# Kernel optimization log

Measured on AMD Instinct MI355X. Metric: run time of the kernel, lower is better.

Reference implementation:

```python
import jax, jax.numpy as jnp
import numpy as np

NUM_HEADS = 16

def setup_inputs() -> dict:
    key = jax.random.key(0)
    ks = jax.random.split(key, 5)
    B, N, C = 2, 2048, 1024
    x = jax.random.normal(ks[0], (B, N, C), dtype=jnp.float32)
    s_in = 1.0 / np.sqrt(C)
    Wq = jax.random.normal(ks[1], (C, 2 * C), dtype=jnp.float32) * s_in
    Wk = jax.random.normal(ks[2], (C, 2 * C), dtype=jnp.float32) * s_in
    Wv = jax.random.normal(ks[3], (C, 2 * C), dtype=jnp.float32) * s_in
    Wo = jax.random.normal(ks[4], (2 * C, C), dtype=jnp.float32) * (1.0 / np.sqrt(2 * C))
    return {"x": x, "Wq": Wq, "Wk": Wk, "Wv": Wv, "Wo": Wo}

def reference(x, Wq, Wk, Wv, Wo):
    B, N, C = x.shape
    H = NUM_HEADS
    hd = C // H  # head_dim
    def proj(W):
        # [B,N,2C] -> [B,H,N,2*hd]
        return (x @ W).reshape(B, N, H, 2 * hd).transpose(0, 2, 1, 3)
    q = proj(Wq)
    k = proj(Wk)
    v = proj(Wv)
    q_r, q_i = q[..., :hd], q[..., hd:]
    k_r, k_i = k[..., :hd], k[..., hd:]
    v_r, v_i = v[..., :hd], v[..., hd:]
    # complex inner product real part: Re(Q K^H) = q_r.k_r + q_i.k_i
    scores = (jnp.einsum('bhnd,bhmd->bhnm', q_r, k_r)
              + jnp.einsum('bhnd,bhmd->bhnm', q_i, k_i)) / jnp.sqrt(jnp.float32(hd))
    causal = jnp.tril(jnp.ones((N, N), dtype=bool))  # [N,N]
    scores = jnp.where(causal[None, None], scores, -jnp.inf)
    probs = jax.nn.softmax(scores, axis=-1)  # dropout off (eval mode)
    out_r = jnp.einsum('bhnm,bhmd->bhnd', probs, v_r)
    out_i = jnp.einsum('bhnm,bhmd->bhnd', probs, v_i)
    out = jnp.concatenate([out_r, out_i], axis=-1)  # [B,H,N,2*hd]
    out = out.transpose(0, 2, 1, 3).reshape(B, N, 2 * C)
    return out @ Wo  # [B,N,C]
```

## Files before the change

kernel.cpp:

```cpp
#include <hip/hip_runtime.h>
#include <hip/hip_bf16.h>
#include <stdint.h>
#include <cmath>

using bf16 = __hip_bfloat16;
typedef __attribute__((ext_vector_type(8))) short bf16x8;
typedef __attribute__((ext_vector_type(4))) short bf16x4;
typedef __attribute__((ext_vector_type(4))) float f32x4;

#define MFMA16(a, b, c) __builtin_amdgcn_mfma_f32_16x16x32_bf16(a, b, c, 0, 0, 0)

#if defined(__has_builtin)
#if __has_builtin(__builtin_amdgcn_mfma_f32_16x16x16bf16_1k)
#define HAVE_MFMA_K16 1
#endif
#if __has_builtin(__builtin_amdgcn_exp2f)
#define EXP2F __builtin_amdgcn_exp2f
#endif
#endif
#ifndef HAVE_MFMA_K16
#define HAVE_MFMA_K16 0
#endif
#ifndef EXP2F
#define EXP2F exp2f
#endif

#define NEG_BIG (-1e30f)
#define K2SCALE 0.18033688011112042f

__device__ __forceinline__ short f2bf(float v) {
  return __builtin_bit_cast(short, __float2bfloat16(v));
}

__device__ __forceinline__ f32x4 pv_mfma(bf16x4 va, bf16x4 pb, f32x4 c) {
#if HAVE_MFMA_K16
  return __builtin_amdgcn_mfma_f32_16x16x16bf16_1k(va, pb, c, 0, 0, 0);
#else
  const bf16x8 a = {va[0], va[1], va[2], va[3], 0, 0, 0, 0};
  const bf16x8 b = {pb[0], pb[1], pb[2], pb[3], 0, 0, 0, 0};
  return MFMA16(a, b, c);
#endif
}

__device__ __forceinline__ void async_ld16(const bf16* g, bf16* l) {
  __builtin_amdgcn_global_load_lds(
      (const __attribute__((address_space(1))) unsigned int*)g,
      (__attribute__((address_space(3))) unsigned int*)l, 16, 0, 0);
}

template <typename T> __device__ __forceinline__ T cvt_out(float v);
template <> __device__ __forceinline__ float cvt_out<float>(float v) { return v; }
template <> __device__ __forceinline__ bf16 cvt_out<bf16>(float v) { return __float2bfloat16(v); }

__global__ void prep(const float* __restrict__ x,
                     const float* __restrict__ Wq, const float* __restrict__ Wk,
                     const float* __restrict__ Wv, const float* __restrict__ Wo,
                     bf16* __restrict__ xb, bf16* __restrict__ tq,
                     bf16* __restrict__ tk, bf16* __restrict__ tv,
                     bf16* __restrict__ to_) {
  __shared__ bf16 tile[32][33];
  const int bid = blockIdx.x;
  if (bid < 8192) {
    const int z = bid >> 11, tt = bid & 2047;
    const float* in = z == 0 ? Wq : z == 1 ? Wk : z == 2 ? Wv : Wo;
    bf16* out = z == 0 ? tq : z == 1 ? tk : z == 2 ? tv : to_;
    int R, Cc, c0, r0;
    if (z < 3) { R = 1024; Cc = 2048; c0 = (tt & 63) * 32; r0 = (tt >> 6) * 32; }
    else       { R = 2048; Cc = 1024; c0 = (tt & 31) * 32; r0 = (tt >> 5) * 32; }
    const int xx = threadIdx.x & 31;
    const int y = threadIdx.x >> 5;
#pragma unroll
    for (int yy = y; yy < 32; yy += 8)
      tile[yy][xx] = __float2bfloat16(in[(size_t)(r0 + yy) * Cc + c0 + xx]);
    __syncthreads();
#pragma unroll
    for (int yy = y; yy < 32; yy += 8)
      out[(size_t)(c0 + yy) * R + r0 + xx] = tile[xx][yy];
  } else {
    const int i = (bid - 8192) * 256 + threadIdx.x;
    const float4 v = ((const float4*)x)[i];
    bf16 o[4] = {__float2bfloat16(v.x), __float2bfloat16(v.y),
                 __float2bfloat16(v.z), __float2bfloat16(v.w)};
    *(uint64_t*)&xb[i * 4] = *(const uint64_t*)o;
  }
}

__global__ __launch_bounds__(256)
void gemm_qkv(const bf16* __restrict__ xb, const bf16* __restrict__ wq,
              const bf16* __restrict__ wk, const bf16* __restrict__ wv,
              bf16* __restrict__ qo, bf16* __restrict__ ko, bf16* __restrict__ vo) {
  __shared__ __align__(16) bf16 As[128 * 64];
  __shared__ __align__(16) bf16 Bs[128 * 64];
  const int op = blockIdx.y;
  const int bid = blockIdx.x;
  const bf16 *A, *B;
  int m0, n0;
  if (op < 2) { A = xb; B = op ? wk : wq; m0 = (bid >> 4) * 128; n0 = (bid & 15) * 128; }
  else        { A = wv; B = xb;           m0 = (bid & 15) * 128; n0 = (bid >> 4) * 128; }
  const int K = 1024;

  const int t = threadIdx.x;
  const int l = t & 63, w = t >> 6;
  const int q4 = l >> 4, li = l & 15;
  const int wr = (w >> 1) * 64, wc = (w & 1) * 64;

  f32x4 acc[4][4] = {};
  const int srow = t >> 3;
  const int schu = t & 7;
  const int wavebase = (t & ~63) * 8;
  const bf16* gA = A + (size_t)m0 * K;
  const bf16* gB = B + (size_t)n0 * K;

  for (int k0 = 0; k0 < K; k0 += 64) {
#pragma unroll
    for (int p = 0; p < 4; ++p) {
      const int row = p * 32 + srow;
      const int cs = (schu ^ (row & 7)) * 8;
      const int lbase = p * 2048 + wavebase;
      async_ld16(gA + (size_t)row * K + k0 + cs, &As[lbase]);
      async_ld16(gB + (size_t)row * K + k0 + cs, &Bs[lbase]);
    }
    __syncthreads();
#pragma unroll
    for (int kk = 0; kk < 2; ++kk) {
      bf16x8 af[4], bfr[4];
#pragma unroll
      for (int i = 0; i < 4; ++i)
        af[i] = *(const bf16x8*)&As[(wr + i * 16 + li) * 64 +
                                    (((kk * 4 + q4) ^ (li & 7)) * 8)];
#pragma unroll
      for (int j = 0; j < 4; ++j)
        bfr[j] = *(const bf16x8*)&Bs[(wc + j * 16 + li) * 64 +
                                     (((kk * 4 + q4) ^ (li & 7)) * 8)];
#pragma unroll
      for (int i = 0; i < 4; ++i)
#pragma unroll
        for (int j = 0; j < 4; ++j)
          acc[i][j] = MFMA16(af[i], bfr[j], acc[i][j]);
    }
    __syncthreads();
  }

#pragma unroll
  for (int i = 0; i < 4; ++i)
#pragma unroll
    for (int j = 0; j < 4; ++j)
#pragma unroll
      for (int r = 0; r < 4; ++r) {
        const int gm = m0 + wr + i * 16 + q4 * 4 + r;
        const int gn = n0 + wc + j * 16 + li;
        const bf16 v = __float2bfloat16(acc[i][j][r]);
        if (op < 2) {
          const int b = gm >> 11, nn = gm & 2047;
          const int h = gn >> 7, d = gn & 127;
          (op ? ko : qo)[((size_t)(b * 16 + h) * 2048 + nn) * 128 + d] = v;
        } else {
          const int h = gm >> 7, d = gm & 127;
          const int b = gn >> 11, nn = gn & 2047;
          vo[((size_t)(b * 16 + h) * 128 + d) * 2048 + nn] = v;
        }
      }
}

template <int NT, typename OT>
__global__ __launch_bounds__(256)
void gemm_bt(const bf16* __restrict__ A, const bf16* __restrict__ B,
             OT* __restrict__ C, int M, int N, int K) {
  __shared__ __align__(16) bf16 As[128 * 32];
  __shared__ __align__(16) bf16 Bs[NT * 32];
  constexpr int JN = NT / 32;
  const int t = threadIdx.x;
  const int l = t & 63, w = t >> 6;
  const int q4 = l >> 4, li = l & 15;
  const int m0 = blockIdx.y * 128;
  const int n0 = blockIdx.x * NT;
  const int wr = (w >> 1) * 64, wc = (w & 1) * (NT / 2);

  f32x4 acc[4][JN] = {};
  const int colst = (t & 3) * 8;
  const bf16* gA = A + (size_t)m0 * K;
  const bf16* gB = B + (size_t)n0 * K;

  for (int k0 = 0; k0 < K; k0 += 32) {
#pragma unroll
    for (int p = 0; p < 2; ++p) {
      const int row = p * 64 + (t >> 2);
      const int lbase = p * 2048 + (t & ~63) * 8;
      async_ld16(gA + (size_t)row * K + k0 + colst, &As[lbase]);
    }
#pragma unroll
    for (int p = 0; p < NT / 64; ++p) {
      const int row = p * 64 + (t >> 2);
      const int lbase = p * 2048 + (t & ~63) * 8;
      async_ld16(gB + (size_t)row * K + k0 + colst, &Bs[lbase]);
    }
    __syncthreads();
    bf16x8 af[4], bfr[JN];
#pragma unroll
    for (int i = 0; i < 4; ++i)
      af[i] = *(const bf16x8*)&As[(wr + i * 16 + li) * 32 + q4 * 8];
#pragma unroll
    for (int j = 0; j < JN; ++j)
      bfr[j] = *(const bf16x8*)&Bs[(wc + j * 16 + li) * 32 + q4 * 8];
#pragma unroll
    for (int i = 0; i < 4; ++i)
#pragma unroll
      for (int j = 0; j < JN; ++j)
        acc[i][j] = MFMA16(af[i], bfr[j], acc[i][j]);
    __syncthreads();
  }

#pragma unroll
  for (int i = 0; i < 4; ++i)
#pragma unroll
    for (int j = 0; j < JN; ++j)
#pragma unroll
      for (int r = 0; r < 4; ++r) {
        const int gm = m0 + wr + i * 16 + q4 * 4 + r;
        const int gn = n0 + wc + j * 16 + li;
        C[(size_t)gm * N + gn] = cvt_out<OT>(acc[i][j][r]);
      }
}

__global__ __launch_bounds__(256, 2)
void flash_attn(const bf16* __restrict__ qm, const bf16* __restrict__ km,
                const bf16* __restrict__ vtm, bf16* __restrict__ om) {
  __shared__ __align__(16) bf16 Ks[64 * 128];
  __shared__ __align__(16) bf16 Vts[128 * 64];

  const int t = threadIdx.x;
  const int l = t & 63, w = t >> 6;
  const int q4 = l >> 4, li = l & 15;
  const int bh = blockIdx.x;
  const int y = blockIdx.y;
  const int qt = (y < 16) ? 31 - y : y - 16;
  const int qs = qt * 64;
  const size_t qkbase = (size_t)bh * 2048 * 128;
  const size_t vbase = (size_t)bh * 128 * 2048;
  const int b = bh >> 4, h = bh & 15;

  bf16x8 qf[4];
  {
    const bf16* Qb = qm + qkbase + (size_t)(qs + w * 16 + li) * 128;
#pragma unroll
    for (int f = 0; f < 4; ++f)
      qf[f] = *(const bf16x8*)(Qb + f * 32 + q4 * 8);
  }

  f32x4 O[8] = {};
  float mrun = NEG_BIG, lrun = 0.f;
  const int gmq = qs + w * 16 + li;

  const int ksrow = t >> 4;
  const int kchu = t & 15;
  const int vsrow = t >> 3;
  const int vchu = t & 7;
  const int wavebase = (t & ~63) * 8;

  const int nt = qt + 1;

  for (int j = 0; j < nt; ++j) {
    const int kb = j * 64;
#pragma unroll
    for (int p = 0; p < 4; ++p) {
      const int kr = p * 16 + ksrow;
      async_ld16(km + qkbase + (size_t)(kb + kr) * 128 + (size_t)((kchu ^ (kr & 7)) * 8),
                 &Ks[p * 2048 + wavebase]);
      const int vr = p * 32 + vsrow;
      async_ld16(vtm + vbase + (size_t)vr * 2048 + kb + (size_t)((vchu ^ (vr & 7)) * 8),
                 &Vts[p * 2048 + wavebase]);
    }
    __syncthreads();

    const bool msk = (j == qt);

    f32x4 S[4];
    __builtin_amdgcn_s_setprio(1);
#pragma unroll
    for (int jk = 0; jk < 4; ++jk) {
      const int krow = jk * 16 + li;
      bf16x8 kf[4];
#pragma unroll
      for (int f = 0; f < 4; ++f)
        kf[f] = *(const bf16x8*)&Ks[krow * 128 + (((f * 4 + q4) ^ (li & 7)) * 8)];
      f32x4 s = {0.f, 0.f, 0.f, 0.f};
#pragma unroll
      for (int f = 0; f < 4; ++f) s = MFMA16(kf[f], qf[f], s);
      S[jk] = s;
    }
    __builtin_amdgcn_s_setprio(0);

    if (msk) {
#pragma unroll
      for (int jk = 0; jk < 4; ++jk)
#pragma unroll
        for (int r = 0; r < 4; ++r)
          if ((kb + jk * 16 + q4 * 4 + r) > gmq) S[jk][r] = NEG_BIG;
    }

    float mx = NEG_BIG;
#pragma unroll
    for (int jk = 0; jk < 4; ++jk)
      mx = fmaxf(mx, fmaxf(fmaxf(S[jk][0], S[jk][1]), fmaxf(S[jk][2], S[jk][3])));
    mx = fmaxf(mx, __shfl_xor(mx, 16));
    mx = fmaxf(mx, __shfl_xor(mx, 32));
    const float mold = mrun;
    const float nm = fmaxf(mrun, mx);
    const bool nomove = (mx <= mold);
    mrun = nm;
    const float nmk = nm * K2SCALE;

    bf16x4 pb[4];
    float rs = 0.f;
#pragma unroll
    for (int jk = 0; jk < 4; ++jk) {
      float e[4];
#pragma unroll
      for (int r = 0; r < 4; ++r) {
        e[r] = EXP2F(__builtin_fmaf(S[jk][r], K2SCALE, -nmk));
        pb[jk][r] = f2bf(e[r]);
      }
      rs += (e[0] + e[1]) + (e[2] + e[3]);
    }
    rs += __shfl_xor(rs, 16);
    rs += __shfl_xor(rs, 32);

    if (__all(nomove)) {
      lrun += rs;
    } else {
      const float alpha = EXP2F((mold - nm) * K2SCALE);
      lrun = lrun * alpha + rs;
#pragma unroll
      for (int dt = 0; dt < 8; ++dt) O[dt] *= alpha;
    }

    __builtin_amdgcn_s_setprio(1);
#pragma unroll
    for (int dt = 0; dt < 8; ++dt)
#pragma unroll
      for (int kc = 0; kc < 4; ++kc) {
        const int gc = kc * 2 + (q4 >> 1);
        const bf16x4 va = *(const bf16x4*)&Vts[(dt * 16 + li) * 64 +
                                               ((gc ^ (li & 7)) * 8) +
                                               (q4 & 1) * 4];
        O[dt] = pv_mfma(va, pb[kc], O[dt]);
      }
    __builtin_amdgcn_s_setprio(0);
    __syncthreads();
  }

  {
    const float inv = 1.0f / lrun;
    const size_t orow = (size_t)(b * 2048 + qs + w * 16 + li) * 2048 + h * 128;
#pragma unroll
    for (int dt = 0; dt < 8; ++dt) {
      bf16x4 o4;
#pragma unroll
      for (int r = 0; r < 4; ++r) o4[r] = f2bf(O[dt][r] * inv);
      *(bf16x4*)&om[orow + dt * 16 + q4 * 4] = o4;
    }
  }
}

extern "C" void kernel_launch(void* const* d_in, const int* in_sizes, int n_in,
                              void* d_out, int out_size, void* d_ws, size_t ws_size,
                              hipStream_t stream) {
  const float* x = (const float*)d_in[0];
  const float* Wq = (const float*)d_in[1];
  const float* Wk = (const float*)d_in[2];
  const float* Wv = (const float*)d_in[3];
  const float* Wo = (const float*)d_in[4];
  float* out = (float*)d_out;

  bf16* ws = (bf16*)d_ws;
  const size_t MEG = 1u << 20;
  bf16* xb = ws;
  bf16* wTq = ws + 4 * MEG;
  bf16* wTk = ws + 6 * MEG;
  bf16* wTv = ws + 8 * MEG;
  bf16* woT = ws + 10 * MEG;
  bf16* at_ws = ws + 2 * MEG;
  bf16* q_ws = ws + 12 * MEG;
  bf16* k_ws = ws + 20 * MEG;
  bf16* vt_ws = ws + 28 * MEG;

  const dim3 blk(256);

  prep<<<dim3(12288), blk, 0, stream>>>(x, Wq, Wk, Wv, Wo, xb, wTq, wTk, wTv, woT);
  gemm_qkv<<<dim3(512, 3), blk, 0, stream>>>(xb, wTq, wTk, wTv, q_ws, k_ws, vt_ws);
  flash_attn<<<dim3(32, 32), blk, 0, stream>>>(q_ws, k_ws, vt_ws, at_ws);
  gemm_bt<64, float><<<dim3(16, 32), blk, 0, stream>>>(at_ws, woT, out, 4096, 1024, 2048);
}
```

Measured before the change: 266.2 us.

## Double K-tile depth in gemm_bt with XOR-swizzled LDS and vectorize prep transpose

The output GEMM kernel now stages 64-wide K slices instead of 32, which halves the number of barrier pairs per K loop. It also XOR-swizzles the 16-byte chunks in LDS to avoid bank conflicts on the fragment reads. The weight-transpose prep kernel now loads float2 and stores packed pairs of bf16 values, so each thread handles two elements. The cost is double the LDS footprint for gemm_bt, which may reduce occupancy.

New measurement: 254.8 us. 1.04x faster.

```diff
diff --git a/kernel.cpp b/kernel.cpp
--- a/kernel.cpp
+++ b/kernel.cpp
@@ -67,15 +67,21 @@
     int R, Cc, c0, r0;
     if (z < 3) { R = 1024; Cc = 2048; c0 = (tt & 63) * 32; r0 = (tt >> 6) * 32; }
     else       { R = 2048; Cc = 1024; c0 = (tt & 31) * 32; r0 = (tt >> 5) * 32; }
-    const int xx = threadIdx.x & 31;
-    const int y = threadIdx.x >> 5;
-#pragma unroll
-    for (int yy = y; yy < 32; yy += 8)
-      tile[yy][xx] = __float2bfloat16(in[(size_t)(r0 + yy) * Cc + c0 + xx]);
-    __syncthreads();
-#pragma unroll
-    for (int yy = y; yy < 32; yy += 8)
-      out[(size_t)(c0 + yy) * R + r0 + xx] = tile[xx][yy];
+    const int xx = threadIdx.x & 15;
+    const int y = threadIdx.x >> 4;
+#pragma unroll
+    for (int yy = y; yy < 32; yy += 16) {
+      const float2 v = *(const float2*)&in[(size_t)(r0 + yy) * Cc + c0 + 2 * xx];
+      tile[yy][2 * xx] = __float2bfloat16(v.x);
+      tile[yy][2 * xx + 1] = __float2bfloat16(v.y);
+    }
+    __syncthreads();
+#pragma unroll
+    for (int yy = y; yy < 32; yy += 16) {
+      short o2[2] = {__builtin_bit_cast(short, tile[2 * xx][yy]),
+                     __builtin_bit_cast(short, tile[2 * xx + 1][yy])};
+      *(uint32_t*)&out[(size_t)(c0 + yy) * R + r0 + 2 * xx] = *(const uint32_t*)o2;
+    }
   } else {
     const int i = (bid - 8192) * 256 + threadIdx.x;
     const float4 v = ((const float4*)x)[i];
@@ -166,8 +172,8 @@
 __global__ __launch_bounds__(256)
 void gemm_bt(const bf16* __restrict__ A, const bf16* __restrict__ B,
              OT* __restrict__ C, int M, int N, int K) {
-  __shared__ __align__(16) bf16 As[128 * 32];
-  __shared__ __align__(16) bf16 Bs[NT * 32];
+  __shared__ __align__(16) bf16 As[128 * 64];
+  __shared__ __align__(16) bf16 Bs[NT * 64];
   constexpr int JN = NT / 32;
   const int t = threadIdx.x;
   const int l = t & 63, w = t >> 6;
@@ -177,36 +183,43 @@
   const int wr = (w >> 1) * 64, wc = (w & 1) * (NT / 2);
 
   f32x4 acc[4][JN] = {};
-  const int colst = (t & 3) * 8;
+  const int srow = t >> 3;
+  const int schu = t & 7;
+  const int wavebase = (t & ~63) * 8;
   const bf16* gA = A + (size_t)m0 * K;
   const bf16* gB = B + (size_t)n0 * K;
 
-  for (int k0 = 0; k0 < K; k0 += 32) {
-#pragma unroll
-    for (int p = 0; p < 2; ++p) {
-      const int row = p * 64 + (t >> 2);
-      const int lbase = p * 2048 + (t & ~63) * 8;
-      async_ld16(gA + (size_t)row * K + k0 + colst, &As[lbase]);
-    }
-#pragma unroll
-    for (int p = 0; p < NT / 64; ++p) {
-      const int row = p * 64 + (t >> 2);
-      const int lbase = p * 2048 + (t & ~63) * 8;
-      async_ld16(gB + (size_t)row * K + k0 + colst, &Bs[lbase]);
-    }
-    __syncthreads();
-    bf16x8 af[4], bfr[JN];
-#pragma unroll
-    for (int i = 0; i < 4; ++i)
-      af[i] = *(const bf16x8*)&As[(wr + i * 16 + li) * 32 + q4 * 8];
-#pragma unroll
-    for (int j = 0; j < JN; ++j)
-      bfr[j] = *(const bf16x8*)&Bs[(wc + j * 16 + li) * 32 + q4 * 8];
-#pragma unroll
-    for (int i = 0; i < 4; ++i)
+  for (int k0 = 0; k0 < K; k0 += 64) {
+#pragma unroll
+    for (int p = 0; p < 4; ++p) {
+      const int row = p * 32 + srow;
+      const int cs = (schu ^ (row & 7)) * 8;
+      async_ld16(gA + (size_t)row * K + k0 + cs, &As[p * 2048 + wavebase]);
+    }
+#pragma unroll
+    for (int p = 0; p < NT / 32; ++p) {
+      const int row = p * 32 + srow;
+      const int cs = (schu ^ (row & 7)) * 8;
+      async_ld16(gB + (size_t)row * K + k0 + cs, &Bs[p * 2048 + wavebase]);
+    }
+    __syncthreads();
+#pragma unroll
+    for (int kk = 0; kk < 2; ++kk) {
+      bf16x8 af[4], bfr[JN];
+#pragma unroll
+      for (int i = 0; i < 4; ++i)
+        af[i] = *(const bf16x8*)&As[(wr + i * 16 + li) * 64 +
+                                    (((kk * 4 + q4) ^ (li & 7)) * 8)];
 #pragma unroll
       for (int j = 0; j < JN; ++j)
-        acc[i][j] = MFMA16(af[i], bfr[j], acc[i][j]);
+        bfr[j] = *(const bf16x8*)&Bs[(wc + j * 16 + li) * 64 +
+                                     (((kk * 4 + q4) ^ (li & 7)) * 8)];
+#pragma unroll
+      for (int i = 0; i < 4; ++i)
+#pragma unroll
+        for (int j = 0; j < JN; ++j)
+          acc[i][j] = MFMA16(af[i], bfr[j], acc[i][j]);
+    }
     __syncthreads();
   }
 
```
